# Optimization experiments

Measured on AMD Instinct MI355X. Metric: run time of the kernel, lower is better.

The kernel has to match this reference:

```python
import jax, jax.numpy as jnp
import numpy as np

BEGIN, END = 32, 543
D_OBJ, D_MODEL = 16, 128
NUM_OBJS = (END - BEGIN + 1) // D_OBJ  # 32
OBS_DIM = 576
BATCH = 32768


def setup_inputs() -> dict:
    key = jax.random.key(0)
    ks = jax.random.split(key, 6)
    def lin_w(k, out_d, in_d):
        b = np.sqrt(6.0 / (in_d + out_d))
        return jax.random.uniform(k, (out_d, in_d), jnp.float32, -b, b)
    obs = jax.random.uniform(ks[0], (BATCH, OBS_DIM), jnp.float32)
    return {
        "obs": obs,
        "W1": lin_w(ks[1], D_MODEL, D_OBJ - 1), "b1": jnp.zeros((D_MODEL,), jnp.float32),
        "W2": lin_w(ks[2], D_MODEL, D_MODEL),   "b2": jnp.zeros((D_MODEL,), jnp.float32),
        "W3": lin_w(ks[3], D_MODEL, D_MODEL),   "b3": jnp.zeros((D_MODEL,), jnp.float32),
        "Uq": lin_w(ks[4], D_MODEL, D_MODEL),
        "Ur": lin_w(ks[5], D_MODEL, D_MODEL),
    }


def reference(obs, W1, b1, W2, b2, W3, b3, Uq, Ur):
    # preprocessing: slice out attention block, keep the rest as auxiliary
    att = obs[:, BEGIN:END + 1]                       # [B, num_objs*d_obj]
    aux = jnp.concatenate([obs[:, :BEGIN], obs[:, END + 1:]], axis=-1)  # [B, 64]

    x = att.reshape(-1, NUM_OBJS, D_OBJ)              # [B, N, d_obj]
    mask = x[:, :, -1]                                # [B, N]
    feats = x[:, :, :-1]                              # [B, N, d_obj-1]

    # 3-layer embedding MLP (Linear -> ReLU -> Linear -> ReLU -> Linear)
    h = jax.nn.relu(jnp.einsum('bnf,df->bnd', feats, W1) + b1)
    h = jax.nn.relu(jnp.einsum('bnd,ed->bne', h, W2) + b2)
    h = jnp.einsum('bnd,ed->bne', h, W3) + b3         # [B, N, d_model]

    x_real = h * mask[..., None]                      # mask out padded objects
    query = x_real.sum(axis=-2) / (mask.sum(axis=-1) + 1e-5)[:, None]  # [B, d_model]

    q = query @ Uq.T                                  # [B, d_model]
    r = jnp.einsum('bnd,ed->bne', x_real, Ur)         # [B, N, d_model]
    logits = jnp.einsum('bd,bnd->bn', q, r) + (1.0 - mask) * (-1e9)
    w = jax.nn.softmax(logits, axis=-1)               # [B, N]
    out_att = jnp.einsum('bn,bnd->bd', w, x_real)     # [B, d_model]

    return jnp.concatenate([aux, out_att], axis=-1)   # [B, 64 + d_model]
```

## Files before the change

kernel.cpp:

```cpp
#include <hip/hip_runtime.h>

typedef __attribute__((ext_vector_type(8))) __bf16 bf16x8;
typedef __attribute__((ext_vector_type(4))) float f32x4;
typedef __attribute__((ext_vector_type(16))) float f32x16;
typedef __attribute__((ext_vector_type(4))) int i32x4;

#define GRID 1024
#define BLOCK 512
#define ITERS 4

__device__ __forceinline__ int swzi(int row, int col) {
    return row * 128 + (col ^ ((row & 7) << 3));
}
__device__ __forceinline__ int cvt_pk_bf16(float lo, float hi) {
    int r; asm("v_cvt_pk_bf16_f32 %0, %1, %2" : "=v"(r) : "v"(lo), "v"(hi)); return r;
}
__device__ __forceinline__ void pl32swap(int& a, int& b) {
    asm("v_permlane32_swap_b32 %0, %1" : "+v"(a), "+v"(b));
}
__device__ __forceinline__ void pl32swapf(float& a, float& b) {
    asm("v_permlane32_swap_b32 %0, %1" : "+v"(a), "+v"(b));
}
__device__ __forceinline__ float bflo(unsigned u) {
    unsigned v = u << 16; return __builtin_bit_cast(float, v);
}
__device__ __forceinline__ float bfhi(unsigned u) {
    unsigned v = u & 0xffff0000u; return __builtin_bit_cast(float, v);
}

__global__ __launch_bounds__(128)
void pack_kernel(const float* __restrict__ W1, const float* __restrict__ b1,
                 const float* __restrict__ W2, const float* __restrict__ W3,
                 const float* __restrict__ Uq, const float* __restrict__ Ur,
                 unsigned char* __restrict__ ws)
{
    __bf16* w1p = (__bf16*)ws;
    __bf16* w2p = (__bf16*)(ws + 4096);
    __bf16* w3p = (__bf16*)(ws + 36864);
    __bf16* mp  = (__bf16*)(ws + 69632);
    const int d = blockIdx.x, t = threadIdx.x;
    if (t < 16) w1p[d * 16 + t] = (__bf16)((t < 15) ? W1[d * 15 + t] : b1[d]);
    w2p[swzi(d, t)] = (__bf16)W2[d * 128 + t];
    w3p[swzi(d, t)] = (__bf16)W3[d * 128 + t];
    float acc = 0.f;
    for (int e = 0; e < 128; ++e)
        acc = fmaf(Ur[e * 128 + d], Uq[e * 128 + t], acc);
    mp[d * 128 + t] = (__bf16)acc;
}

__global__ __launch_bounds__(BLOCK, 2)
void fused_attn_kernel(const float* __restrict__ obs,
                       const float* __restrict__ b2g, const float* __restrict__ b3g,
                       const unsigned char* __restrict__ ws,
                       float* __restrict__ out)
{
    const __bf16* gW1 = (const __bf16*)ws;
    const __bf16* gW2 = (const __bf16*)(ws + 4096);
    const __bf16* gW3 = (const __bf16*)(ws + 36864);
    const __bf16* gM  = (const __bf16*)(ws + 69632);

    __shared__ __align__(16) __bf16 sW2[128 * 128];
    __shared__ __align__(16) __bf16 sW3[128 * 128];
    __shared__ __align__(16) __bf16 sX[256 * 128];
    __shared__ __align__(16) __bf16 sQ[16 * 128];
    __shared__ __align__(16) float sV[8 * 128];
    __shared__ __align__(16) float sB2[128], sB3[128];

    const int tid = threadIdx.x, lane = tid & 63, wv = tid >> 6;
    const int l31 = lane & 31, hi = lane >> 5;
    const int l15 = lane & 15, kh = lane >> 4;

    for (int i = tid * 8; i < 128 * 128; i += BLOCK * 8) {
        *(bf16x8*)&sW2[i] = *(const bf16x8*)&gW2[i];
        *(bf16x8*)&sW3[i] = *(const bf16x8*)&gW3[i];
    }
    for (int i = tid; i < 16 * 128; i += BLOCK) sQ[i] = (__bf16)0.f;
    if (tid < 128) { sB2[tid] = b2g[tid]; sB3[tid] = b3g[tid]; }

    bf16x8 w1f[4];
    #pragma unroll
    for (int m = 0; m < 4; ++m)
        w1f[m] = *(const bf16x8*)&gW1[(m * 32 + l31) * 16 + hi * 8];
    bf16x8 mf[4];
    #pragma unroll
    for (int kk = 0; kk < 4; ++kk)
        mf[kk] = *(const bf16x8*)&gM[(wv * 16 + l15) * 128 + kk * 32 + kh * 8];
    __syncthreads();

    auto layer32 = [&](const f32x16 (&src)[4], f32x16 (&dst)[4],
                       const __bf16* Ws, const float* sB, bool do_relu) {
        #pragma unroll
        for (int m = 0; m < 4; ++m) {
            f32x16 z;
            #pragma unroll
            for (int r = 0; r < 16; ++r) z[r] = 0.f;
            dst[m] = z;
        }
        #pragma unroll
        for (int kt = 0; kt < 8; ++kt) {
            const int ms = kt >> 1, b0 = (kt & 1) * 8;
            int Pa0 = cvt_pk_bf16(src[ms][b0 + 0], src[ms][b0 + 1]);
            int Pb0 = cvt_pk_bf16(src[ms][b0 + 2], src[ms][b0 + 3]);
            int Pa1 = cvt_pk_bf16(src[ms][b0 + 4], src[ms][b0 + 5]);
            int Pb1 = cvt_pk_bf16(src[ms][b0 + 6], src[ms][b0 + 7]);
            pl32swap(Pa0, Pa1);
            pl32swap(Pb0, Pb1);
            i32x4 wi; wi.x = Pa0; wi.y = Pb0; wi.z = Pa1; wi.w = Pb1;
            bf16x8 bfr = __builtin_bit_cast(bf16x8, wi);
            #pragma unroll
            for (int m = 0; m < 4; ++m) {
                int row = m * 32 + l31;
                bf16x8 afr = *(const bf16x8*)&Ws[row * 128 + ((kt * 16 + hi * 8) ^ ((row & 7) << 3))];
                dst[m] = __builtin_amdgcn_mfma_f32_32x32x16_bf16(afr, bfr, dst[m], 0, 0, 0);
            }
        }
        #pragma unroll
        for (int m = 0; m < 4; ++m)
            #pragma unroll
            for (int rg = 0; rg < 4; ++rg) {
                f32x4 bb = *(const f32x4*)&sB[m * 32 + rg * 8 + hi * 4];
                #pragma unroll
                for (int r = 0; r < 4; ++r) {
                    float v = dst[m][rg * 4 + r] + bb[r];
                    dst[m][rg * 4 + r] = do_relu ? fmaxf(v, 0.f) : v;
                }
            }
    };

    for (int g = 0; g < ITERS; ++g) {
        const int row0 = blockIdx.x * (8 * ITERS) + g * 8;
        const int rb   = row0 + wv;
        const int xrow = wv * 32;

        f32x16 acc1[4], acc2[4];
        float mk, rden;

        {
            const float* src = &obs[(size_t)rb * 576 + 32 + l31 * 16 + hi * 8];
            f32x4 u0 = *(const f32x4*)src;
            f32x4 u1 = *(const f32x4*)(src + 4);
            float maskv = 0.f;
            if (hi) { maskv = u1.w; u1.w = 1.0f; }
            bf16x8 bfr;
            bfr[0] = (__bf16)u0.x; bfr[1] = (__bf16)u0.y;
            bfr[2] = (__bf16)u0.z; bfr[3] = (__bf16)u0.w;
            bfr[4] = (__bf16)u1.x; bfr[5] = (__bf16)u1.y;
            bfr[6] = (__bf16)u1.z; bfr[7] = (__bf16)u1.w;
            float ma = maskv, mb = maskv;
            pl32swapf(ma, mb);
            mk = hi ? maskv : mb;
            float s = mk;
            s += __shfl_xor(s, 1);  s += __shfl_xor(s, 2);
            s += __shfl_xor(s, 4);  s += __shfl_xor(s, 8);
            s += __shfl_xor(s, 16);
            rden = 1.f / (s + 1e-5f);

            #pragma unroll
            for (int m = 0; m < 4; ++m) {
                f32x16 z;
                #pragma unroll
                for (int r = 0; r < 16; ++r) z[r] = 0.f;
                acc1[m] = __builtin_amdgcn_mfma_f32_32x32x16_bf16(w1f[m], bfr, z, 0, 0, 0);
                #pragma unroll
                for (int r = 0; r < 16; ++r) acc1[m][r] = fmaxf(acc1[m][r], 0.f);
            }
        }

        layer32(acc1, acc2, sW2, sB2, true);
        layer32(acc2, acc1, sW3, sB3, false);

        #pragma unroll
        for (int m = 0; m < 4; ++m)
            #pragma unroll
            for (int r = 0; r < 16; ++r) acc1[m][r] *= mk;

        #pragma unroll
        for (int m = 0; m < 4; ++m)
            #pragma unroll
            for (int rg = 0; rg < 4; ++rg) {
                int pk0 = cvt_pk_bf16(acc1[m][rg * 4 + 0], acc1[m][rg * 4 + 1]);
                int pk1 = cvt_pk_bf16(acc1[m][rg * 4 + 2], acc1[m][rg * 4 + 3]);
                int e0 = m * 32 + rg * 8 + hi * 4;
                int row = xrow + l31;
                int2 pp; pp.x = pk0; pp.y = pk1;
                *(int2*)&sX[row * 128 + (e0 ^ ((row & 7) << 3))] = pp;
            }

        {
            float s0 = 0.f, s1 = 0.f;
            #pragma unroll
            for (int i = 0; i < 32; ++i) {
                int row = xrow + i;
                unsigned u = *(const unsigned*)&sX[row * 128 + ((2 * lane) ^ ((i & 7) << 3))];
                s0 += bflo(u); s1 += bfhi(u);
            }
            int qpk = cvt_pk_bf16(s0 * rden, s1 * rden);
            *(unsigned*)&sQ[wv * 128 + ((2 * lane) ^ (wv << 3))] = (unsigned)qpk;
            float av = (lane < 32) ? obs[(size_t)rb * 576 + lane]
                                   : obs[(size_t)rb * 576 + 512 + lane];
            out[(size_t)rb * 192 + lane] = av;
        }
        __syncthreads();

        {
            f32x4 vac = {0.f, 0.f, 0.f, 0.f};
            #pragma unroll
            for (int kk = 0; kk < 4; ++kk) {
                bf16x8 a = *(const bf16x8*)&sQ[l15 * 128 + ((kk * 32 + kh * 8) ^ ((l15 & 7) << 3))];
                vac = __builtin_amdgcn_mfma_f32_16x16x32_bf16(a, mf[kk], vac, 0, 0, 0);
            }
            if (kh < 2) {
                #pragma unroll
                for (int r = 0; r < 4; ++r)
                    sV[(kh * 4 + r) * 128 + wv * 16 + l15] = vac[r];
            }
        }
        __syncthreads();

        {
            float lp = 0.f;
            #pragma unroll
            for (int m = 0; m < 4; ++m)
                #pragma unroll
                for (int rg = 0; rg < 4; ++rg) {
                    f32x4 vv = *(const f32x4*)&sV[wv * 128 + m * 32 + rg * 8 + hi * 4];
                    #pragma unroll
                    for (int r = 0; r < 4; ++r) lp = fmaf(vv[r], acc1[m][rg * 4 + r], lp);
                }
            float la = lp, lb = lp;
            pl32swapf(la, lb);
            float lpo = hi ? la : lb;
            float logit = lp + lpo + (1.f - mk) * (-1e9f);
            float mx = logit;
            mx = fmaxf(mx, __shfl_xor(mx, 1));  mx = fmaxf(mx, __shfl_xor(mx, 2));
            mx = fmaxf(mx, __shfl_xor(mx, 4));  mx = fmaxf(mx, __shfl_xor(mx, 8));
            mx = fmaxf(mx, __shfl_xor(mx, 16));
            float ex = __expf(logit - mx);
            float ss = ex;
            ss += __shfl_xor(ss, 1);  ss += __shfl_xor(ss, 2);
            ss += __shfl_xor(ss, 4);  ss += __shfl_xor(ss, 8);
            ss += __shfl_xor(ss, 16);
            float w = ex / ss;

            float o0 = 0.f, o1 = 0.f;
            int wb = __builtin_bit_cast(int, w);
            #pragma unroll
            for (int i = 0; i < 32; ++i) {
                float wi = __builtin_bit_cast(float, __builtin_amdgcn_readlane(wb, i));
                int row = xrow + i;
                unsigned u = *(const unsigned*)&sX[row * 128 + ((2 * lane) ^ ((i & 7) << 3))];
                o0 = fmaf(wi, bflo(u), o0);
                o1 = fmaf(wi, bfhi(u), o1);
            }
            float2 o; o.x = o0; o.y = o1;
            *(float2*)&out[(size_t)rb * 192 + 64 + 2 * lane] = o;
        }
    }
}

extern "C" void kernel_launch(void* const* d_in, const int* in_sizes, int n_in,
                              void* d_out, int out_size, void* d_ws, size_t ws_size,
                              hipStream_t stream) {
    const float* obs = (const float*)d_in[0];
    const float* W1  = (const float*)d_in[1];
    const float* b1  = (const float*)d_in[2];
    const float* W2  = (const float*)d_in[3];
    const float* b2  = (const float*)d_in[4];
    const float* W3  = (const float*)d_in[5];
    const float* b3  = (const float*)d_in[6];
    const float* Uq  = (const float*)d_in[7];
    const float* Ur  = (const float*)d_in[8];
    float* out = (float*)d_out;
    unsigned char* ws = (unsigned char*)d_ws;

    pack_kernel<<<dim3(128), dim3(128), 0, stream>>>(W1, b1, W2, W3, Uq, Ur, ws);
    fused_attn_kernel<<<dim3(GRID), dim3(BLOCK), 0, stream>>>(
        obs, b2, b3, ws, out);
}
```

Measured before the change: 111.6 us.

## Prefetch next obs rows, double-buffer weight fragments, split accumulators, add MFMA priority

The layer function now seeds accumulators with the bias, keeping only the ReLU after the loop. It also loads each k-step's weight fragments from LDS one step ahead of the MFMAs. The next iteration's observation row is prefetched into registers while the current one is processed. Serial reduction chains (query sum, logit dot, output weighting) are split into several partial accumulators for more ILP, and s_setprio brackets the MFMA groups. These aim to hide LDS and global latency at the cost of extra registers and possible occupancy pressure.

```diff
diff --git a/kernel.cpp b/kernel.cpp
--- a/kernel.cpp
+++ b/kernel.cpp
@@ -90,14 +90,29 @@
     auto layer32 = [&](const f32x16 (&src)[4], f32x16 (&dst)[4],
                        const __bf16* Ws, const float* sB, bool do_relu) {
         #pragma unroll
+        for (int m = 0; m < 4; ++m)
+            #pragma unroll
+            for (int rg = 0; rg < 4; ++rg) {
+                f32x4 bb = *(const f32x4*)&sB[m * 32 + rg * 8 + hi * 4];
+                dst[m][rg * 4 + 0] = bb.x; dst[m][rg * 4 + 1] = bb.y;
+                dst[m][rg * 4 + 2] = bb.z; dst[m][rg * 4 + 3] = bb.w;
+            }
+        bf16x8 af[4];
+        #pragma unroll
         for (int m = 0; m < 4; ++m) {
-            f32x16 z;
-            #pragma unroll
-            for (int r = 0; r < 16; ++r) z[r] = 0.f;
-            dst[m] = z;
+            int row = m * 32 + l31;
+            af[m] = *(const bf16x8*)&Ws[row * 128 + ((hi * 8) ^ ((row & 7) << 3))];
         }
         #pragma unroll
         for (int kt = 0; kt < 8; ++kt) {
+            bf16x8 afn[4];
+            if (kt < 7) {
+                #pragma unroll
+                for (int m = 0; m < 4; ++m) {
+                    int row = m * 32 + l31;
+                    afn[m] = *(const bf16x8*)&Ws[row * 128 + (((kt + 1) * 16 + hi * 8) ^ ((row & 7) << 3))];
+                }
+            }
             const int ms = kt >> 1, b0 = (kt & 1) * 8;
             int Pa0 = cvt_pk_bf16(src[ms][b0 + 0], src[ms][b0 + 1]);
             int Pb0 = cvt_pk_bf16(src[ms][b0 + 2], src[ms][b0 + 3]);
@@ -107,25 +122,31 @@
             pl32swap(Pb0, Pb1);
             i32x4 wi; wi.x = Pa0; wi.y = Pb0; wi.z = Pa1; wi.w = Pb1;
             bf16x8 bfr = __builtin_bit_cast(bf16x8, wi);
-            #pragma unroll
-            for (int m = 0; m < 4; ++m) {
-                int row = m * 32 + l31;
-                bf16x8 afr = *(const bf16x8*)&Ws[row * 128 + ((kt * 16 + hi * 8) ^ ((row & 7) << 3))];
-                dst[m] = __builtin_amdgcn_mfma_f32_32x32x16_bf16(afr, bfr, dst[m], 0, 0, 0);
-            }
-        }
-        #pragma unroll
-        for (int m = 0; m < 4; ++m)
-            #pragma unroll
-            for (int rg = 0; rg < 4; ++rg) {
-                f32x4 bb = *(const f32x4*)&sB[m * 32 + rg * 8 + hi * 4];
-                #pragma unroll
-                for (int r = 0; r < 4; ++r) {
-                    float v = dst[m][rg * 4 + r] + bb[r];
-                    dst[m][rg * 4 + r] = do_relu ? fmaxf(v, 0.f) : v;
-                }
-            }
+            __builtin_amdgcn_s_setprio(1);
+            #pragma unroll
+            for (int m = 0; m < 4; ++m)
+                dst[m] = __builtin_amdgcn_mfma_f32_32x32x16_bf16(af[m], bfr, dst[m], 0, 0, 0);
+            __builtin_amdgcn_s_setprio(0);
+            if (kt < 7) {
+                #pragma unroll
+                for (int m = 0; m < 4; ++m) af[m] = afn[m];
+            }
+        }
+        if (do_relu) {
+            #pragma unroll
+            for (int m = 0; m < 4; ++m)
+                #pragma unroll
+                for (int r = 0; r < 16; ++r)
+                    dst[m][r] = fmaxf(dst[m][r], 0.f);
+        }
     };
+
+    f32x4 pu0, pu1;
+    {
+        const float* s0 = &obs[(size_t)(blockIdx.x * (8 * ITERS) + wv) * 576 + 32 + l31 * 16 + hi * 8];
+        pu0 = *(const f32x4*)s0;
+        pu1 = *(const f32x4*)(s0 + 4);
+    }
 
     for (int g = 0; g < ITERS; ++g) {
         const int row0 = blockIdx.x * (8 * ITERS) + g * 8;
@@ -136,9 +157,7 @@
         float mk, rden;
 
         {
-            const float* src = &obs[(size_t)rb * 576 + 32 + l31 * 16 + hi * 8];
-            f32x4 u0 = *(const f32x4*)src;
-            f32x4 u1 = *(const f32x4*)(src + 4);
+            f32x4 u0 = pu0, u1 = pu1;
             float maskv = 0.f;
             if (hi) { maskv = u1.w; u1.w = 1.0f; }
             bf16x8 bfr;
@@ -155,24 +174,32 @@
             s += __shfl_xor(s, 16);
             rden = 1.f / (s + 1e-5f);
 
-            #pragma unroll
-            for (int m = 0; m < 4; ++m) {
-                f32x16 z;
-                #pragma unroll
-                for (int r = 0; r < 16; ++r) z[r] = 0.f;
+            f32x16 z;
+            #pragma unroll
+            for (int r = 0; r < 16; ++r) z[r] = 0.f;
+            __builtin_amdgcn_s_setprio(1);
+            #pragma unroll
+            for (int m = 0; m < 4; ++m)
                 acc1[m] = __builtin_amdgcn_mfma_f32_32x32x16_bf16(w1f[m], bfr, z, 0, 0, 0);
-                #pragma unroll
-                for (int r = 0; r < 16; ++r) acc1[m][r] = fmaxf(acc1[m][r], 0.f);
-            }
+            __builtin_amdgcn_s_setprio(0);
+
+            if (g + 1 < ITERS) {
+                const float* sn = &obs[(size_t)(rb + 8) * 576 + 32 + l31 * 16 + hi * 8];
+                pu0 = *(const f32x4*)sn;
+                pu1 = *(const f32x4*)(sn + 4);
+            }
+            #pragma unroll
+            for (int m = 0; m < 4; ++m)
+                #pragma unroll
+                for (int r = 0; r < 16; ++r)
+                    acc1[m][r] = fmaxf(acc1[m][r], 0.f);
         }
 
         layer32(acc1, acc2, sW2, sB2, true);
         layer32(acc2, acc1, sW3, sB3, false);
 
         #pragma unroll
-        for (int m = 0; m < 4; ++m)
-            #pragma unroll
-            for (int r = 0; r < 16; ++r) acc1[m][r] *= mk;
+        for (int m = 0; m < 4; ++m) acc1[m] = acc1[m] * mk;
 
         #pragma unroll
         for (int m = 0; m < 4; ++m)
@@ -187,13 +214,16 @@
             }
 
         {
-            float s0 = 0.f, s1 = 0.f;
+            float s0p[4] = {0.f, 0.f, 0.f, 0.f}, s1p[4] = {0.f, 0.f, 0.f, 0.f};
             #pragma unroll
             for (int i = 0; i < 32; ++i) {
                 int row = xrow + i;
                 unsigned u = *(const unsigned*)&sX[row * 128 + ((2 * lane) ^ ((i & 7) << 3))];
-                s0 += bflo(u); s1 += bfhi(u);
-            }
+                s0p[i & 3] += bflo(u);
+                s1p[i & 3] += bfhi(u);
+            }
+            float s0 = (s0p[0] + s0p[1]) + (s0p[2] + s0p[3]);
+            float s1 = (s1p[0] + s1p[1]) + (s1p[2] + s1p[3]);
             int qpk = cvt_pk_bf16(s0 * rden, s1 * rden);
             *(unsigned*)&sQ[wv * 128 + ((2 * lane) ^ (wv << 3))] = (unsigned)qpk;
             float av = (lane < 32) ? obs[(size_t)rb * 576 + lane]
@@ -204,11 +234,13 @@
 
         {
             f32x4 vac = {0.f, 0.f, 0.f, 0.f};
+            __builtin_amdgcn_s_setprio(1);
             #pragma unroll
             for (int kk = 0; kk < 4; ++kk) {
                 bf16x8 a = *(const bf16x8*)&sQ[l15 * 128 + ((kk * 32 + kh * 8) ^ ((l15 & 7) << 3))];
                 vac = __builtin_amdgcn_mfma_f32_16x16x32_bf16(a, mf[kk], vac, 0, 0, 0);
             }
+            __builtin_amdgcn_s_setprio(0);
             if (kh < 2) {
                 #pragma unroll
                 for (int r = 0; r < 4; ++r)
@@ -218,15 +250,17 @@
         __syncthreads();
 
         {
-            float lp = 0.f;
+            float lpm[4] = {0.f, 0.f, 0.f, 0.f};
             #pragma unroll
             for (int m = 0; m < 4; ++m)
                 #pragma unroll
                 for (int rg = 0; rg < 4; ++rg) {
                     f32x4 vv = *(const f32x4*)&sV[wv * 128 + m * 32 + rg * 8 + hi * 4];
                     #pragma unroll
-                    for (int r = 0; r < 4; ++r) lp = fmaf(vv[r], acc1[m][rg * 4 + r], lp);
+                    for (int r = 0; r < 4; ++r)
+                        lpm[m] = fmaf(vv[r], acc1[m][rg * 4 + r], lpm[m]);
                 }
+            float lp = (lpm[0] + lpm[1]) + (lpm[2] + lpm[3]);
             float la = lp, lb = lp;
             pl32swapf(la, lb);
             float lpo = hi ? la : lb;
@@ -242,17 +276,17 @@
             ss += __shfl_xor(ss, 16);
             float w = ex / ss;
 
-            float o0 = 0.f, o1 = 0.f;
+            float o0p[2] = {0.f, 0.f}, o1p[2] = {0.f, 0.f};
             int wb = __builtin_bit_cast(int, w);
             #pragma unroll
             for (int i = 0; i < 32; ++i) {
                 float wi = __builtin_bit_cast(float, __builtin_amdgcn_readlane(wb, i));
                 int row = xrow + i;
                 unsigned u = *(const unsigned*)&sX[row * 128 + ((2 * lane) ^ ((i & 7) << 3))];
-                o0 = fmaf(wi, bflo(u), o0);
-                o1 = fmaf(wi, bfhi(u), o1);
-            }
-            float2 o; o.x = o0; o.y = o1;
+                o0p[i & 1] = fmaf(wi, bflo(u), o0p[i & 1]);
+                o1p[i & 1] = fmaf(wi, bfhi(u), o1p[i & 1]);
+            }
+            float2 o; o.x = o0p[0] + o0p[1]; o.y = o1p[0] + o1p[1];
             *(float2*)&out[(size_t)rb * 192 + 64 + 2 * lane] = o;
         }
     }
```

New measurement: 135.7 us, median of 2. +21.6%, slower.
